# Kernel tuning notes

Measured on AMD Instinct MI355X. Metric: run time of the kernel, lower is better.

The kernel has to match this reference:

```python
import jax, jax.numpy as jnp
import numpy as np

B, N, QDIM = 2, 4096, 768
H, D = 8, 64  # num_head, head_dim; inner_dim = 512
INNER = H * D


def setup_inputs() -> dict:
    key = jax.random.key(0)
    ks = jax.random.split(key, 6)
    s = lambda fan_in: 1.0 / np.sqrt(fan_in)
    return {
        "x": jax.random.normal(ks[0], (B, N, QDIM), dtype=jnp.float32),
        "Wq": jax.random.normal(ks[1], (QDIM, INNER), dtype=jnp.float32) * s(QDIM),
        "Wk": jax.random.normal(ks[2], (QDIM, INNER), dtype=jnp.float32) * s(QDIM),
        "Wv": jax.random.normal(ks[3], (QDIM, INNER), dtype=jnp.float32) * s(QDIM),
        "Wout": jax.random.normal(ks[4], (INNER, QDIM), dtype=jnp.float32) * s(INNER),
        "b_out": jnp.zeros((QDIM,), dtype=jnp.float32),
    }


def reference(x, Wq, Wk, Wv, Wout, b_out):
    # x: [b, n, q_dim]; self-attention (kv = x), no mask, dropout = 0 (eval).
    scale = D ** -0.5
    # project and split heads: [b, n, h*d] -> [b, h, n, d]
    def heads(t):
        b, n, _ = t.shape
        return t.reshape(b, n, H, D).transpose(0, 2, 1, 3)
    q = heads(x @ Wq)
    k = heads(x @ Wk)
    v = heads(x @ Wv)
    qk = jnp.einsum("bhid,bhjd->bhij", q, k) * scale  # [b, h, n, n] -- O(n^2) matrix
    attn = jax.nn.softmax(qk, axis=-1)
    out = jnp.einsum("bhij,bhjd->bhid", attn, v)  # [b, h, n, d]
    out = out.transpose(0, 2, 1, 3).reshape(x.shape[0], x.shape[1], INNER)
    return out @ Wout + b_out
```

## Files before the change

### kernel.cpp

```cpp
#include <hip/hip_runtime.h>
#include <cstdint>
#include <cstddef>


typedef __attribute__((ext_vector_type(8))) short short8;
typedef __attribute__((ext_vector_type(4))) float f32x4;

__device__ __forceinline__ unsigned short f2bf(float f) {
  unsigned int u = __float_as_uint(f);
  u = (u + 0x7fffu + ((u >> 16) & 1u)) >> 16;
  return (unsigned short)u;
}

__device__ __forceinline__ float fast_exp2(float x) {
#if __has_builtin(__builtin_amdgcn_exp2f)
  return __builtin_amdgcn_exp2f(x);
#else
  return __expf(x * 0.69314718055994531f);
#endif
}

__device__ __forceinline__ void gld16(const void* g, void* l) {
  __builtin_amdgcn_global_load_lds(
      (__attribute__((address_space(1))) void*)const_cast<void*>(g),
      (__attribute__((address_space(3))) void*)l, 16, 0, 0);
}


__global__ __launch_bounds__(256) void cvt_x_k(const float* __restrict__ x,
                                               unsigned short* __restrict__ xb) {
  const size_t i = ((size_t)blockIdx.x * 256 + threadIdx.x) * 4;
  const float4 v = *(const float4*)(x + i);
  ushort4 u;
  u.x = f2bf(v.x); u.y = f2bf(v.y); u.z = f2bf(v.z); u.w = f2bf(v.w);
  *(ushort4*)(xb + i) = u;
}

__global__ __launch_bounds__(256) void transpose_w_k(
    const float* __restrict__ Wq, const float* __restrict__ Wk,
    const float* __restrict__ Wv, const float* __restrict__ Wout,
    unsigned short* __restrict__ Wt,
    unsigned short* __restrict__ WoT)
{
  __shared__ float t[32][33];
  const int z = blockIdx.z;
  const float* src = (z == 0) ? Wq : (z == 1) ? Wk : (z == 2) ? Wv : Wout;
  const int R = (z < 3) ? 768 : 512, C = (z < 3) ? 512 : 768;
  unsigned short* dst = (z < 3) ? (Wt + (size_t)z * 393216) : WoT;
  const int tx = threadIdx.x & 31, ty = threadIdx.x >> 5;
  const int c0 = blockIdx.x * 32, r0 = blockIdx.y * 32;
  if (c0 >= C || r0 >= R) return;
#pragma unroll
  for (int k = 0; k < 4; ++k)
    t[ty + 8 * k][tx] = src[(size_t)(r0 + ty + 8 * k) * C + c0 + tx];
  __syncthreads();
#pragma unroll
  for (int k = 0; k < 4; ++k)
    dst[(size_t)(c0 + ty + 8 * k) * R + r0 + tx] = f2bf(t[tx][ty + 8 * k]);
}


__global__ __launch_bounds__(256) void gemm_qkv_k(
    const unsigned short* __restrict__ A,
    const unsigned short* __restrict__ Wt,
    unsigned short* __restrict__ qb, unsigned short* __restrict__ kb,
    unsigned short* __restrict__ vtb) {
  __shared__ __align__(16) short Al[4096];
  __shared__ __align__(16) short Bl[4096];
  const int tid = threadIdx.x;
  const int w = tid >> 6, lane = tid & 63, quad = lane >> 4, l15 = lane & 15;
  const int wy = w >> 1, wx = w & 1;
  const int m0 = blockIdx.x * 128, n0 = blockIdx.y * 128;
  const int z = blockIdx.z;
  const unsigned short* Bt = Wt + (size_t)z * (512 * 768);

  f32x4 acc[4][4];
#pragma unroll
  for (int i = 0; i < 4; ++i)
#pragma unroll
    for (int j = 0; j < 4; ++j) acc[i][j] = (f32x4){0.f, 0.f, 0.f, 0.f};

  for (int k0 = 0; k0 < 768; k0 += 32) {
    __syncthreads();
#pragma unroll
    for (int s = 0; s < 2; ++s) {
      const int t = s * 256 + tid;
      gld16(A + (size_t)(m0 + (t >> 2)) * 768 + k0 + (t & 3) * 8,
            Al + s * 2048 + w * 512);
      gld16(Bt + (size_t)(n0 + (t >> 2)) * 768 + k0 + (t & 3) * 8,
            Bl + s * 2048 + w * 512);
    }
    __syncthreads();
    short8 af[4], bf[4];
#pragma unroll
    for (int i = 0; i < 4; ++i) {
      af[i] = *(const short8*)(Al + (wy * 64 + i * 16 + l15) * 32 + quad * 8);
      bf[i] = *(const short8*)(Bl + (wx * 64 + i * 16 + l15) * 32 + quad * 8);
    }
    if (z == 2) {
#pragma unroll
      for (int i = 0; i < 4; ++i)
#pragma unroll
        for (int j = 0; j < 4; ++j)
          acc[i][j] = __builtin_amdgcn_mfma_f32_16x16x32_bf16(bf[i], af[j], acc[i][j], 0, 0, 0);
    } else {
#pragma unroll
      for (int i = 0; i < 4; ++i)
#pragma unroll
        for (int j = 0; j < 4; ++j)
          acc[i][j] = __builtin_amdgcn_mfma_f32_16x16x32_bf16(af[i], bf[j], acc[i][j], 0, 0, 0);
    }
  }

#pragma unroll
  for (int i = 0; i < 4; ++i) {
#pragma unroll
    for (int j = 0; j < 4; ++j) {
#pragma unroll
      for (int r = 0; r < 4; ++r) {
        if (z == 2) {
          const int n = n0 + wx * 64 + i * 16 + quad * 4 + r;
          const int m = m0 + wy * 64 + j * 16 + l15;
          const int b = m >> 12, nseq = m & 4095;
          const int h = n >> 6, d = n & 63;
          vtb[(size_t)((b * 8 + h) * 64 + d) * 4096 + nseq] = f2bf(acc[i][j][r]);
        } else {
          const int m = m0 + wy * 64 + i * 16 + quad * 4 + r;
          const int col = n0 + wx * 64 + j * 16 + l15;
          const int b = m >> 12, nseq = m & 4095;
          const int h = col >> 6, d = col & 63;
          const int bh = b * 8 + h;
          if (z == 0) {
            qb[(size_t)(bh * 4096 + nseq) * 64 + d] =
                f2bf(acc[i][j][r] * 0.18033688011112042f);
          } else {
            kb[(size_t)(bh * 4096 + nseq) * 64 + d] = f2bf(acc[i][j][r]);
          }
        }
      }
    }
  }
}


__global__ __launch_bounds__(512) void attn_k(
    const unsigned short* __restrict__ qb,
    const unsigned short* __restrict__ kb,
    const unsigned short* __restrict__ vtb,
    unsigned short* __restrict__ ob) {
  __shared__ __align__(16) char smem[65536];
  short* Kl = (short*)smem;
  short* Vl = (short*)(smem + 16384);
  short* Pl = (short*)(smem + 32768);

  const int tid = threadIdx.x;
  const int w = tid >> 6, lane = tid & 63, quad = lane >> 4, l15 = lane & 15;
  const int g = w >> 2, wq = w & 3;
  const int tg = tid & 255;
  const int bh = blockIdx.y;
  const int q0 = blockIdx.x * 128;
  const unsigned short* qbase = qb + (size_t)bh * 4096 * 64;
  const unsigned short* kbase = kb + (size_t)bh * 4096 * 64;
  const unsigned short* vbase = vtb + (size_t)bh * 64 * 4096;
  short* pw = Pl + w * 2048;
  const int jbase = g * 2048;
  const int e8 = l15 & 7;

  short8 qf[2][2];
#pragma unroll
  for (int qh = 0; qh < 2; ++qh) {
    const int qrow = q0 + wq * 32 + qh * 16 + l15;
    qf[qh][0] = *(const short8*)(qbase + (size_t)qrow * 64 + quad * 8);
    qf[qh][1] = *(const short8*)(qbase + (size_t)qrow * 64 + 32 + quad * 8);
  }

  const short one_bf = (short)0x3F80;
  const short8 vones = {one_bf, one_bf, one_bf, one_bf,
                        one_bf, one_bf, one_bf, one_bf};

  f32x4 Oacc[2][4];
#pragma unroll
  for (int qh = 0; qh < 2; ++qh)
#pragma unroll
    for (int nf = 0; nf < 4; ++nf) Oacc[qh][nf] = (f32x4){0.f, 0.f, 0.f, 0.f};
  f32x4 Lacc[2] = {(f32x4){0.f, 0.f, 0.f, 0.f}, (f32x4){0.f, 0.f, 0.f, 0.f}};

  for (int j0 = 0; j0 < 2048; j0 += 64) {
    const int jj = jbase + j0;
    __syncthreads();
#pragma unroll
    for (int c = 0; c < 2; ++c) {
      gld16(kbase + (size_t)(jj + (tg >> 2)) * 64 + c * 32 + (tg & 3) * 8,
            Kl + ((g * 2 + c) * 64 + wq * 16) * 32);
      gld16(vbase + (size_t)(tg >> 2) * 4096 + jj + c * 32 + (tg & 3) * 8,
            Vl + ((g * 2 + c) * 64 + wq * 16) * 32);
    }
    __syncthreads();

#pragma unroll
    for (int kt = 0; kt < 4; ++kt) {
      const short8 ka0 = *(const short8*)(Kl + ((g * 2 + 0) * 64 + kt * 16 + l15) * 32 + quad * 8);
      const short8 ka1 = *(const short8*)(Kl + ((g * 2 + 1) * 64 + kt * 16 + l15) * 32 + quad * 8);
#pragma unroll
      for (int qh = 0; qh < 2; ++qh) {
        f32x4 st = (f32x4){0.f, 0.f, 0.f, 0.f};
        st = __builtin_amdgcn_mfma_f32_16x16x32_bf16(ka0, qf[qh][0], st, 0, 0, 0);
        st = __builtin_amdgcn_mfma_f32_16x16x32_bf16(ka1, qf[qh][1], st, 0, 0, 0);
        const unsigned int u0 = __float_as_uint(fast_exp2(st[0]));
        const unsigned int u1 = __float_as_uint(fast_exp2(st[1]));
        const unsigned int u2 = __float_as_uint(fast_exp2(st[2]));
        const unsigned int u3 = __float_as_uint(fast_exp2(st[3]));
        uint2 pd;
        pd.x = (u1 & 0xFFFF0000u) | (u0 >> 16);
        pd.y = (u3 & 0xFFFF0000u) | (u2 >> 16);
        *(uint2*)(pw + (qh * 16 + l15) * 64 +
                  (((2 * kt + (quad >> 1)) ^ e8) * 8 + (quad & 1) * 4)) = pd;
      }
    }

    asm volatile("s_waitcnt lgkmcnt(0)" ::: "memory");

#pragma unroll
    for (int c = 0; c < 2; ++c) {
      short8 pa[2];
#pragma unroll
      for (int qh = 0; qh < 2; ++qh)
        pa[qh] = *(const short8*)(pw + (qh * 16 + l15) * 64 +
                                  ((4 * c + quad) ^ e8) * 8);
#pragma unroll
      for (int nf = 0; nf < 4; ++nf) {
        const short8 vb = *(const short8*)(Vl + ((g * 2 + c) * 64 + nf * 16 + l15) * 32 + quad * 8);
#pragma unroll
        for (int qh = 0; qh < 2; ++qh)
          Oacc[qh][nf] = __builtin_amdgcn_mfma_f32_16x16x32_bf16(
              pa[qh], vb, Oacc[qh][nf], 0, 0, 0);
      }
#pragma unroll
      for (int qh = 0; qh < 2; ++qh)
        Lacc[qh] = __builtin_amdgcn_mfma_f32_16x16x32_bf16(pa[qh], vones, Lacc[qh], 0, 0, 0);
    }
  }

  __syncthreads();
  float* Ox = (float*)smem;
  float* Lx = (float*)(smem + 33280);
  if (g == 1) {
#pragma unroll
    for (int qh = 0; qh < 2; ++qh)
#pragma unroll
      for (int r = 0; r < 4; ++r) {
        const int row = wq * 32 + qh * 16 + quad * 4 + r;
        Lx[row] = Lacc[qh][r];
#pragma unroll
        for (int nf = 0; nf < 4; ++nf)
          Ox[row * 65 + nf * 16 + l15] = Oacc[qh][nf][r];
      }
  }
  __syncthreads();
  if (g == 0) {
    const int b = bh >> 3, h = bh & 7;
#pragma unroll
    for (int qh = 0; qh < 2; ++qh)
#pragma unroll
      for (int r = 0; r < 4; ++r) {
        const int rl = wq * 32 + qh * 16 + quad * 4 + r;
        const float inv = 1.0f / (Lacc[qh][r] + Lx[rl]);
        const int row = q0 + rl;
#pragma unroll
        for (int nf = 0; nf < 4; ++nf)
          ob[(size_t)(b * 4096 + row) * 512 + h * 64 + nf * 16 + l15] =
              f2bf((Oacc[qh][nf][r] + Ox[rl * 65 + nf * 16 + l15]) * inv);
      }
  }
}


__global__ __launch_bounds__(256) void gemm_out_k(
    const unsigned short* __restrict__ A,
    const unsigned short* __restrict__ Bt,
    const float* __restrict__ bias, float* __restrict__ out) {
  __shared__ __align__(16) short Al[4096];
  __shared__ __align__(16) short Bl[2048];
  const int tid = threadIdx.x;
  const int w = tid >> 6, lane = tid & 63, quad = lane >> 4, l15 = lane & 15;
  const int m0 = blockIdx.x * 128, n0 = blockIdx.y * 64;

  f32x4 acc[2][4];
#pragma unroll
  for (int i = 0; i < 2; ++i)
#pragma unroll
    for (int j = 0; j < 4; ++j) acc[i][j] = (f32x4){0.f, 0.f, 0.f, 0.f};

  for (int k0 = 0; k0 < 512; k0 += 32) {
    __syncthreads();
#pragma unroll
    for (int s = 0; s < 2; ++s) {
      const int t = s * 256 + tid;
      gld16(A + (size_t)(m0 + (t >> 2)) * 512 + k0 + (t & 3) * 8,
            Al + s * 2048 + w * 512);
    }
    gld16(Bt + (size_t)(n0 + (tid >> 2)) * 512 + k0 + (tid & 3) * 8,
          Bl + w * 512);
    __syncthreads();
    short8 af[2], bf[4];
#pragma unroll
    for (int i = 0; i < 2; ++i)
      af[i] = *(const short8*)(Al + (w * 32 + i * 16 + l15) * 32 + quad * 8);
#pragma unroll
    for (int j = 0; j < 4; ++j)
      bf[j] = *(const short8*)(Bl + (j * 16 + l15) * 32 + quad * 8);
#pragma unroll
    for (int i = 0; i < 2; ++i)
#pragma unroll
      for (int j = 0; j < 4; ++j)
        acc[i][j] = __builtin_amdgcn_mfma_f32_16x16x32_bf16(af[i], bf[j], acc[i][j], 0, 0, 0);
  }

#pragma unroll
  for (int i = 0; i < 2; ++i) {
#pragma unroll
    for (int j = 0; j < 4; ++j) {
#pragma unroll
      for (int r = 0; r < 4; ++r) {
        const int m = m0 + w * 32 + i * 16 + quad * 4 + r;
        const int col = n0 + j * 16 + l15;
        out[(size_t)m * 768 + col] = acc[i][j][r] + bias[col];
      }
    }
  }
}


extern "C" void kernel_launch(void* const* d_in, const int* in_sizes, int n_in,
                              void* d_out, int out_size, void* d_ws, size_t ws_size,
                              hipStream_t stream) {
  const float* x    = (const float*)d_in[0];
  const float* Wq   = (const float*)d_in[1];
  const float* Wk   = (const float*)d_in[2];
  const float* Wv   = (const float*)d_in[3];
  const float* Wout = (const float*)d_in[4];
  const float* bout = (const float*)d_in[5];
  float* out = (float*)d_out;
  char* ws = (char*)d_ws;

  unsigned short* xb  = (unsigned short*)(ws);
  unsigned short* Wt  = (unsigned short*)(ws + 12582912);
  unsigned short* WoT = (unsigned short*)(ws + 14942208);
  unsigned short* qb  = (unsigned short*)(ws + 15728640);
  unsigned short* kb  = (unsigned short*)(ws + 24117248);
  unsigned short* vtb = (unsigned short*)(ws + 32505856);
  unsigned short* ob  = (unsigned short*)(ws + 40894464);

  cvt_x_k<<<6144, 256, 0, stream>>>(x, xb);
  transpose_w_k<<<dim3(24, 24, 4), 256, 0, stream>>>(Wq, Wk, Wv, Wout, Wt, WoT);
  gemm_qkv_k<<<dim3(64, 4, 3), 256, 0, stream>>>(xb, Wt, qb, kb, vtb);
  attn_k<<<dim3(32, 16), 512, 0, stream>>>(qb, kb, vtb, ob);
  gemm_out_k<<<dim3(64, 12), 256, 0, stream>>>(ob, WoT, bout, out);
}
```

Measured before the change: 241.2 us.

## Vectorize GEMM epilogue stores and enlarge per-wave query tile in attention

The QKV and output GEMMs swap MFMA operand order so each lane holds four consecutive output columns, and write them as ushort4/float4 vector stores instead of scalar stores. The attention kernel goes from 512 to 256 threads per block, with each wave handling 64 query rows instead of 32. This lets each K/V fragment read from LDS feed twice as many MFMAs. The cost is more accumulator registers per wave and fewer waves per block to hide latency.

```diff
diff --git a/kernel.cpp b/kernel.cpp
--- a/kernel.cpp
+++ b/kernel.cpp
@@ -102,40 +102,50 @@
       for (int i = 0; i < 4; ++i)
 #pragma unroll
         for (int j = 0; j < 4; ++j)
+          acc[i][j] = __builtin_amdgcn_mfma_f32_16x16x32_bf16(af[i], bf[j], acc[i][j], 0, 0, 0);
+    } else {
+#pragma unroll
+      for (int i = 0; i < 4; ++i)
+#pragma unroll
+        for (int j = 0; j < 4; ++j)
           acc[i][j] = __builtin_amdgcn_mfma_f32_16x16x32_bf16(bf[i], af[j], acc[i][j], 0, 0, 0);
-    } else {
-#pragma unroll
-      for (int i = 0; i < 4; ++i)
-#pragma unroll
-        for (int j = 0; j < 4; ++j)
-          acc[i][j] = __builtin_amdgcn_mfma_f32_16x16x32_bf16(af[i], bf[j], acc[i][j], 0, 0, 0);
-    }
-  }
-
-#pragma unroll
-  for (int i = 0; i < 4; ++i) {
-#pragma unroll
-    for (int j = 0; j < 4; ++j) {
-#pragma unroll
-      for (int r = 0; r < 4; ++r) {
-        if (z == 2) {
-          const int n = n0 + wx * 64 + i * 16 + quad * 4 + r;
-          const int m = m0 + wy * 64 + j * 16 + l15;
-          const int b = m >> 12, nseq = m & 4095;
-          const int h = n >> 6, d = n & 63;
-          vtb[(size_t)((b * 8 + h) * 64 + d) * 4096 + nseq] = f2bf(acc[i][j][r]);
+    }
+  }
+
+  if (z == 2) {
+#pragma unroll
+    for (int i = 0; i < 4; ++i) {
+#pragma unroll
+      for (int j = 0; j < 4; ++j) {
+        const int m0r = m0 + wy * 64 + i * 16 + quad * 4;
+        const int n = n0 + wx * 64 + j * 16 + l15;
+        const int b = m0r >> 12, nseq0 = m0r & 4095;
+        const int h = n >> 6, d = n & 63;
+        ushort4 u;
+        u.x = f2bf(acc[i][j][0]); u.y = f2bf(acc[i][j][1]);
+        u.z = f2bf(acc[i][j][2]); u.w = f2bf(acc[i][j][3]);
+        *(ushort4*)(vtb + (size_t)((b * 8 + h) * 64 + d) * 4096 + nseq0) = u;
+      }
+    }
+  } else {
+    const float qs = 0.18033688011112042f;
+#pragma unroll
+    for (int i = 0; i < 4; ++i) {
+#pragma unroll
+      for (int j = 0; j < 4; ++j) {
+        const int n0r = n0 + wx * 64 + i * 16 + quad * 4;
+        const int m = m0 + wy * 64 + j * 16 + l15;
+        const int b = m >> 12, nseq = m & 4095;
+        const int h = n0r >> 6, d0 = n0r & 63;
+        ushort4 u;
+        if (z == 0) {
+          u.x = f2bf(acc[i][j][0] * qs); u.y = f2bf(acc[i][j][1] * qs);
+          u.z = f2bf(acc[i][j][2] * qs); u.w = f2bf(acc[i][j][3] * qs);
+          *(ushort4*)(qb + (size_t)((b * 8 + h) * 4096 + nseq) * 64 + d0) = u;
         } else {
-          const int m = m0 + wy * 64 + i * 16 + quad * 4 + r;
-          const int col = n0 + wx * 64 + j * 16 + l15;
-          const int b = m >> 12, nseq = m & 4095;
-          const int h = col >> 6, d = col & 63;
-          const int bh = b * 8 + h;
-          if (z == 0) {
-            qb[(size_t)(bh * 4096 + nseq) * 64 + d] =
-                f2bf(acc[i][j][r] * 0.18033688011112042f);
-          } else {
-            kb[(size_t)(bh * 4096 + nseq) * 64 + d] = f2bf(acc[i][j][r]);
-          }
+          u.x = f2bf(acc[i][j][0]); u.y = f2bf(acc[i][j][1]);
+          u.z = f2bf(acc[i][j][2]); u.w = f2bf(acc[i][j][3]);
+          *(ushort4*)(kb + (size_t)((b * 8 + h) * 4096 + nseq) * 64 + d0) = u;
         }
       }
     }
@@ -143,7 +153,7 @@
 }
 
 
-__global__ __launch_bounds__(512) void attn_k(
+__global__ __launch_bounds__(256) void attn_k(
     const unsigned short* __restrict__ qb,
     const unsigned short* __restrict__ kb,
     const unsigned short* __restrict__ vtb,
@@ -155,21 +165,22 @@
 
   const int tid = threadIdx.x;
   const int w = tid >> 6, lane = tid & 63, quad = lane >> 4, l15 = lane & 15;
-  const int g = w >> 2, wq = w & 3;
-  const int tg = tid & 255;
+  const int g = w >> 1, wq = w & 1;
   const int bh = blockIdx.y;
   const int q0 = blockIdx.x * 128;
   const unsigned short* qbase = qb + (size_t)bh * 4096 * 64;
   const unsigned short* kbase = kb + (size_t)bh * 4096 * 64;
   const unsigned short* vbase = vtb + (size_t)bh * 64 * 4096;
-  short* pw = Pl + w * 2048;
+  short* pw = Pl + w * 4096;
+  short* KlG = Kl + g * 4096;
+  short* VlG = Vl + g * 4096;
   const int jbase = g * 2048;
   const int e8 = l15 & 7;
 
-  short8 qf[2][2];
-#pragma unroll
-  for (int qh = 0; qh < 2; ++qh) {
-    const int qrow = q0 + wq * 32 + qh * 16 + l15;
+  short8 qf[4][2];
+#pragma unroll
+  for (int qh = 0; qh < 4; ++qh) {
+    const int qrow = q0 + wq * 64 + qh * 16 + l15;
     qf[qh][0] = *(const short8*)(qbase + (size_t)qrow * 64 + quad * 8);
     qf[qh][1] = *(const short8*)(qbase + (size_t)qrow * 64 + 32 + quad * 8);
   }
@@ -178,31 +189,37 @@
   const short8 vones = {one_bf, one_bf, one_bf, one_bf,
                         one_bf, one_bf, one_bf, one_bf};
 
-  f32x4 Oacc[2][4];
-#pragma unroll
-  for (int qh = 0; qh < 2; ++qh)
+  f32x4 Oacc[4][4];
+#pragma unroll
+  for (int qh = 0; qh < 4; ++qh)
 #pragma unroll
     for (int nf = 0; nf < 4; ++nf) Oacc[qh][nf] = (f32x4){0.f, 0.f, 0.f, 0.f};
-  f32x4 Lacc[2] = {(f32x4){0.f, 0.f, 0.f, 0.f}, (f32x4){0.f, 0.f, 0.f, 0.f}};
+  f32x4 Lacc[4];
+#pragma unroll
+  for (int qh = 0; qh < 4; ++qh) Lacc[qh] = (f32x4){0.f, 0.f, 0.f, 0.f};
 
   for (int j0 = 0; j0 < 2048; j0 += 64) {
     const int jj = jbase + j0;
     __syncthreads();
 #pragma unroll
     for (int c = 0; c < 2; ++c) {
-      gld16(kbase + (size_t)(jj + (tg >> 2)) * 64 + c * 32 + (tg & 3) * 8,
-            Kl + ((g * 2 + c) * 64 + wq * 16) * 32);
-      gld16(vbase + (size_t)(tg >> 2) * 4096 + jj + c * 32 + (tg & 3) * 8,
-            Vl + ((g * 2 + c) * 64 + wq * 16) * 32);
+#pragma unroll
+      for (int hf = 0; hf < 2; ++hf) {
+        const int row = wq * 32 + hf * 16;
+        gld16(kbase + (size_t)(jj + row + (lane >> 2)) * 64 + c * 32 + (lane & 3) * 8,
+              KlG + (c * 64 + row) * 32);
+        gld16(vbase + (size_t)(row + (lane >> 2)) * 4096 + jj + c * 32 + (lane & 3) * 8,
+              VlG + (c * 64 + row) * 32);
+      }
     }
     __syncthreads();
 
 #pragma unroll
     for (int kt = 0; kt < 4; ++kt) {
-      const short8 ka0 = *(const short8*)(Kl + ((g * 2 + 0) * 64 + kt * 16 + l15) * 32 + quad * 8);
-      const short8 ka1 = *(const short8*)(Kl + ((g * 2 + 1) * 64 + kt * 16 + l15) * 32 + quad * 8);
-#pragma unroll
-      for (int qh = 0; qh < 2; ++qh) {
+      const short8 ka0 = *(const short8*)(KlG + (0 * 64 + kt * 16 + l15) * 32 + quad * 8);
+      const short8 ka1 = *(const short8*)(KlG + (1 * 64 + kt * 16 + l15) * 32 + quad * 8);
+#pragma unroll
+      for (int qh = 0; qh < 4; ++qh) {
         f32x4 st = (f32x4){0.f, 0.f, 0.f, 0.f};
         st = __builtin_amdgcn_mfma_f32_16x16x32_bf16(ka0, qf[qh][0], st, 0, 0, 0);
         st = __builtin_amdgcn_mfma_f32_16x16x32_bf16(ka1, qf[qh][1], st, 0, 0, 0);
@@ -222,21 +239,21 @@
 
 #pragma unroll
     for (int c = 0; c < 2; ++c) {
-      short8 pa[2];
-#pragma unroll
-      for (int qh = 0; qh < 2; ++qh)
+      short8 pa[4];
+#pragma unroll
+      for (int qh = 0; qh < 4; ++qh)
         pa[qh] = *(const short8*)(pw + (qh * 16 + l15) * 64 +
                                   ((4 * c + quad) ^ e8) * 8);
 #pragma unroll
       for (int nf = 0; nf < 4; ++nf) {
-        const short8 vb = *(const short8*)(Vl + ((g * 2 + c) * 64 + nf * 16 + l15) * 32 + quad * 8);
-#pragma unroll
-        for (int qh = 0; qh < 2; ++qh)
+        const short8 vb = *(const short8*)(VlG + (c * 64 + nf * 16 + l15) * 32 + quad * 8);
+#pragma unroll
+        for (int qh = 0; qh < 4; ++qh)
           Oacc[qh][nf] = __builtin_amdgcn_mfma_f32_16x16x32_bf16(
               pa[qh], vb, Oacc[qh][nf], 0, 0, 0);
       }
 #pragma unroll
-      for (int qh = 0; qh < 2; ++qh)
+      for (int qh = 0; qh < 4; ++qh)
         Lacc[qh] = __builtin_amdgcn_mfma_f32_16x16x32_bf16(pa[qh], vones, Lacc[qh], 0, 0, 0);
     }
   }
@@ -246,24 +263,24 @@
   float* Lx = (float*)(smem + 33280);
   if (g == 1) {
 #pragma unroll
-    for (int qh = 0; qh < 2; ++qh)
+    for (int qh = 0; qh < 4; ++qh)
 #pragma unroll
       for (int r = 0; r < 4; ++r) {
-        const int row = wq * 32 + qh * 16 + quad * 4 + r;
-        Lx[row] = Lacc[qh][r];
+        const int rl = wq * 64 + qh * 16 + quad * 4 + r;
+        Lx[rl] = Lacc[qh][r];
 #pragma unroll
         for (int nf = 0; nf < 4; ++nf)
-          Ox[row * 65 + nf * 16 + l15] = Oacc[qh][nf][r];
+          Ox[rl * 65 + nf * 16 + l15] = Oacc[qh][nf][r];
       }
   }
   __syncthreads();
   if (g == 0) {
     const int b = bh >> 3, h = bh & 7;
 #pragma unroll
-    for (int qh = 0; qh < 2; ++qh)
+    for (int qh = 0; qh < 4; ++qh)
 #pragma unroll
       for (int r = 0; r < 4; ++r) {
-        const int rl = wq * 32 + qh * 16 + quad * 4 + r;
+        const int rl = wq * 64 + qh * 16 + quad * 4 + r;
         const float inv = 1.0f / (Lacc[qh][r] + Lx[rl]);
         const int row = q0 + rl;
 #pragma unroll
@@ -313,19 +330,20 @@
     for (int i = 0; i < 2; ++i)
 #pragma unroll
       for (int j = 0; j < 4; ++j)
-        acc[i][j] = __builtin_amdgcn_mfma_f32_16x16x32_bf16(af[i], bf[j], acc[i][j], 0, 0, 0);
+        acc[i][j] = __builtin_amdgcn_mfma_f32_16x16x32_bf16(bf[j], af[i], acc[i][j], 0, 0, 0);
   }
 
 #pragma unroll
   for (int i = 0; i < 2; ++i) {
 #pragma unroll
     for (int j = 0; j < 4; ++j) {
-#pragma unroll
-      for (int r = 0; r < 4; ++r) {
-        const int m = m0 + w * 32 + i * 16 + quad * 4 + r;
-        const int col = n0 + j * 16 + l15;
-        out[(size_t)m * 768 + col] = acc[i][j][r] + bias[col];
-      }
+      const int col0 = n0 + j * 16 + quad * 4;
+      const int m = m0 + w * 32 + i * 16 + l15;
+      const float4 b4 = *(const float4*)(bias + col0);
+      float4 o;
+      o.x = acc[i][j][0] + b4.x; o.y = acc[i][j][1] + b4.y;
+      o.z = acc[i][j][2] + b4.z; o.w = acc[i][j][3] + b4.w;
+      *(float4*)(out + (size_t)m * 768 + col0) = o;
     }
   }
 }
@@ -354,6 +372,6 @@
   cvt_x_k<<<6144, 256, 0, stream>>>(x, xb);
   transpose_w_k<<<dim3(24, 24, 4), 256, 0, stream>>>(Wq, Wk, Wv, Wout, Wt, WoT);
   gemm_qkv_k<<<dim3(64, 4, 3), 256, 0, stream>>>(xb, Wt, qb, kb, vtb);
-  attn_k<<<dim3(32, 16), 512, 0, stream>>>(qb, kb, vtb, ob);
+  attn_k<<<dim3(32, 16), 256, 0, stream>>>(qb, kb, vtb, ob);
   gemm_out_k<<<dim3(64, 12), 256, 0, stream>>>(ob, WoT, bout, out);
 }
```

Result: no change. 240.7 us (-0.2%).
